# Kernel optimization log

Measured on AMD Instinct MI355X. Metric: run time of the kernel, lower is better.

Reference implementation:

```python
import jax, jax.numpy as jnp
import numpy as np

ALPHA = 1.702
LIMIT = 7.0
TOP_K = 2
B, S, H, E, I = 2, 1024, 768, 8, 768


def setup_inputs() -> dict:
    key = jax.random.key(0)
    ks = jax.random.split(key, 7)
    scale = 0.02
    return {
        "hidden_states": jax.random.normal(ks[0], (B, S, H), dtype=jnp.float32),
        "Wr": jax.random.normal(ks[1], (H, E), dtype=jnp.float32) * scale,
        "br": jax.random.normal(ks[2], (E,), dtype=jnp.float32) * scale,
        "Wgu": jax.random.normal(ks[3], (E, H, 2 * I), dtype=jnp.float32) * scale,
        "bgu": jax.random.normal(ks[4], (E, 2 * I), dtype=jnp.float32) * scale,
        "Wd": jax.random.normal(ks[5], (E, I, H), dtype=jnp.float32) * scale,
        "bd": jax.random.normal(ks[6], (E, H), dtype=jnp.float32) * scale,
    }


def reference(hidden_states, Wr, br, Wgu, bgu, Wd, bd):
    # Router: top-K experts per token, softmax over the K selected logits
    logits = jnp.einsum("bsh,he->bse", hidden_states, Wr) + br
    topk_vals, topk_idx = jax.lax.top_k(logits, TOP_K)        # [B,S,K]
    router_scores = jax.nn.softmax(topk_vals, axis=-1)         # [B,S,K]

    # Dense-over-experts grouped GEMM (sparse_matmul reference: unselected
    # experts are computed but never read by the combine gather below).
    gu = jnp.einsum("bsh,ehf->bsef", hidden_states, Wgu) + bgu  # [B,S,E,2I]
    gu = jnp.minimum(gu, LIMIT)
    gate = gu[..., :I]
    up = jnp.maximum(gu[..., I:], -LIMIT)
    glu = gate * jax.nn.sigmoid(gate * ALPHA)
    activated = (up + 1.0) * glu                                # [B,S,E,I]

    down = jnp.einsum("bsei,eih->bseh", activated, Wd) + bd     # [B,S,E,H]

    # all_to_all_combine (num_devices=1): gather this token's K expert outputs
    sel = jnp.take_along_axis(down, topk_idx[..., None], axis=2)  # [B,S,K,H]
    output = jnp.sum(sel * router_scores[..., None], axis=2)      # [B,S,H]
    return output
```

## Files before the change

kernel.cpp:

```cpp
#include <hip/hip_runtime.h>
#include <hip/hip_bf16.h>
#include <cmath>

#define ALPHA 1.702f
#define LIMIT 7.0f

constexpr int B = 2, S = 1024, H = 768, E = 8, I = 768;
constexpr int T = B * S;
constexpr int TWO_I = 2 * I;
constexpr int CAP = T;
constexpr int NROWS = T * 2;
constexpr int NT1 = I / 64;
constexpr int NT2 = H / 64;
constexpr int MT = CAP / 128;

typedef __attribute__((ext_vector_type(8))) short short8;
typedef __attribute__((ext_vector_type(4))) float floatx4;

__device__ __forceinline__ unsigned short f2bf(float v) {
  __hip_bfloat16 h = __float2bfloat16(v);
  return *reinterpret_cast<unsigned short*>(&h);
}

__device__ __forceinline__ void g2l16(const void* g, void* l) {
  __builtin_amdgcn_global_load_lds(
      (const __attribute__((address_space(1))) void*)g,
      (__attribute__((address_space(3))) void*)l, 16, 0, 0);
}

__global__ __launch_bounds__(64) void router_kernel(
    const float* __restrict__ x, const float* __restrict__ Wr,
    const float* __restrict__ br, int* __restrict__ topk_idx,
    float* __restrict__ topk_w, unsigned short* __restrict__ xb,
    float* __restrict__ out) {
  int t = blockIdx.x;
  int lane = threadIdx.x;
  const float* xr = x + (size_t)t * H;

  float4 z4 = {0.f, 0.f, 0.f, 0.f};
#pragma unroll
  for (int j = 0; j < 3; j++)
    *(float4*)(out + (size_t)t * H + (size_t)(j * 64 + lane) * 4) = z4;

  float acc[E];
#pragma unroll
  for (int e = 0; e < E; e++) acc[e] = 0.0f;

#pragma unroll
  for (int it = 0; it < 3; it++) {
    int h4 = it * 64 + lane;
    float4 xv = *(const float4*)(xr + (size_t)h4 * 4);
    ushort4 xo;
    xo.x = f2bf(xv.x);
    xo.y = f2bf(xv.y);
    xo.z = f2bf(xv.z);
    xo.w = f2bf(xv.w);
    *(ushort4*)(xb + (size_t)t * H + (size_t)h4 * 4) = xo;
    const float* wrow = Wr + (size_t)h4 * 4 * E;
    float xs[4] = {xv.x, xv.y, xv.z, xv.w};
#pragma unroll
    for (int j = 0; j < 4; j++)
#pragma unroll
      for (int e = 0; e < E; e++) acc[e] += xs[j] * wrow[j * E + e];
  }
#pragma unroll
  for (int e = 0; e < E; e++) {
    float v = acc[e];
    for (int off = 32; off > 0; off >>= 1) v += __shfl_down(v, off, 64);
    acc[e] = v;
  }
  if (lane == 0) {
    float logits[E];
#pragma unroll
    for (int e = 0; e < E; e++) logits[e] = acc[e] + br[e];
    int i0 = 0;
    float v0 = logits[0];
#pragma unroll
    for (int e = 1; e < E; e++)
      if (logits[e] > v0) { v0 = logits[e]; i0 = e; }
    int i1 = -1;
    float v1 = -INFINITY;
#pragma unroll
    for (int e = 0; e < E; e++) {
      if (e == i0) continue;
      if (logits[e] > v1) { v1 = logits[e]; i1 = e; }
    }
    float s1 = __expf(v1 - v0);
    float denom = 1.0f + s1;
    topk_idx[t * 2 + 0] = i0;
    topk_idx[t * 2 + 1] = i1;
    topk_w[t * 2 + 0] = 1.0f / denom;
    topk_w[t * 2 + 1] = s1 / denom;
  }
}

__global__ __launch_bounds__(256) void transpose_all(
    const float* __restrict__ Wgu, const float* __restrict__ Wd,
    unsigned short* __restrict__ Wgt, unsigned short* __restrict__ Wdt,
    const int* __restrict__ topk_idx, const float* __restrict__ topk_w,
    int* __restrict__ e_cnt, int* __restrict__ row_token,
    float* __restrict__ row_w) {
  int z = blockIdx.z;
  int tid = threadIdx.x;

  if (z == 16) {
    if (blockIdx.x != 0 || blockIdx.y != 0) return;
    __shared__ int cur[E];
    if (tid < E) cur[tid] = 0;
    __syncthreads();
    for (int i = tid; i < NROWS; i += 256) {
      int e = topk_idx[i];
      int pos = atomicAdd(&cur[e], 1);
      row_token[e * CAP + pos] = i >> 1;
      row_w[e * CAP + pos] = topk_w[i];
    }
    __syncthreads();
    if (tid < E) e_cnt[tid] = cur[tid];
    return;
  }

  int which = z >> 3, e = z & 7;
  int N = which ? H : TWO_I;
  if (which && blockIdx.x >= (H / 64)) return;
  const float* in = which ? (Wd + (size_t)e * H * I)
                          : (Wgu + (size_t)e * H * TWO_I);
  unsigned short* out = which ? (Wdt + (size_t)e * H * I)
                              : (Wgt + (size_t)e * H * TWO_I);
  constexpr int K = 768;
  int n0 = blockIdx.x * 64, k0 = blockIdx.y * 64;

  __shared__ float tile[64][65];
  int jr = tid & 15, r0 = tid >> 4;
#pragma unroll
  for (int p = 0; p < 4; p++) {
    int k = r0 + p * 16;
    float4 v = *(const float4*)(in + (size_t)(k0 + k) * N + n0 + jr * 4);
    tile[k][jr * 4 + 0] = v.x;
    tile[k][jr * 4 + 1] = v.y;
    tile[k][jr * 4 + 2] = v.z;
    tile[k][jr * 4 + 3] = v.w;
  }
  __syncthreads();
#pragma unroll
  for (int p = 0; p < 4; p++) {
    int n = r0 + p * 16;
    ushort4 o;
    o.x = f2bf(tile[jr * 4 + 0][n]);
    o.y = f2bf(tile[jr * 4 + 1][n]);
    o.z = f2bf(tile[jr * 4 + 2][n]);
    o.w = f2bf(tile[jr * 4 + 3][n]);
    *(ushort4*)(out + (size_t)(n0 + n) * K + k0 + jr * 4) = o;
  }
}

__global__ __launch_bounds__(256) void gemm_gu_mfma(
    const unsigned short* __restrict__ xb, const unsigned short* __restrict__ Wgt,
    const float* __restrict__ bgu, const int* __restrict__ e_cnt,
    const int* __restrict__ row_token, unsigned short* __restrict__ act) {
  int bid = blockIdx.x;
  int g = bid % (E * NT1);
  int mt = bid / (E * NT1);
  int e = g / NT1;
  int n0 = (g % NT1) * 64;
  int cnt = e_cnt[e];
  int m0 = mt * 128;
  if (m0 >= cnt) return;
  int start = e * CAP;
  const unsigned short* Wg = Wgt + (size_t)e * TWO_I * H;
  const float* bias = bgu + (size_t)e * TWO_I;

  __shared__ short As[2][128 * 64];
  __shared__ short Bg[2][64 * 64];
  __shared__ short Bu[2][64 * 64];
  __shared__ int tok[128];

  int tid = threadIdx.x;
  if (tid < 128) {
    int m = m0 + tid;
    tok[tid] = row_token[start + ((m < cnt) ? m : (cnt - 1))];
  }
  __syncthreads();

  int lane = tid & 63;
  int wave = tid >> 6;
  int quad = lane >> 4;
  int lrow = lane & 15;
  int wm = (wave >> 1) * 64;
  int wn = (wave & 1) * 32;

  const unsigned short* gA[4];
  int oA[4];
#pragma unroll
  for (int r = 0; r < 4; r++) {
    int s = (wave * 4 + r) * 64 + lane;
    int row = s >> 3;
    int gg = (s & 7) ^ (row & 7);
    gA[r] = xb + (size_t)tok[row] * H + gg * 8;
    oA[r] = (wave * 4 + r) * 64 * 8;
  }
  const unsigned short *gBg[2], *gBu[2];
  int oB[2];
#pragma unroll
  for (int r = 0; r < 2; r++) {
    int s = (wave * 2 + r) * 64 + lane;
    int row = s >> 3;
    int gg = (s & 7) ^ (row & 7);
    gBg[r] = Wg + (size_t)(n0 + row) * H + gg * 8;
    gBu[r] = gBg[r] + (size_t)I * H;
    oB[r] = (wave * 2 + r) * 64 * 8;
  }

  float bgv[2], buv[2];
#pragma unroll
  for (int tj = 0; tj < 2; tj++) {
    int ncol = n0 + wn + tj * 16 + lrow;
    bgv[tj] = bias[ncol];
    buv[tj] = bias[I + ncol];
  }

  floatx4 accg[4][2], accu[4][2];
#pragma unroll
  for (int i = 0; i < 4; i++)
#pragma unroll
    for (int j = 0; j < 2; j++) {
      accg[i][j] = floatx4{0.f, 0.f, 0.f, 0.f};
      accu[i][j] = floatx4{0.f, 0.f, 0.f, 0.f};
    }

  __syncthreads();

#pragma unroll
  for (int r = 0; r < 4; r++) g2l16(gA[r], &As[0][oA[r]]);
#pragma unroll
  for (int r = 0; r < 2; r++) {
    g2l16(gBg[r], &Bg[0][oB[r]]);
    g2l16(gBu[r], &Bu[0][oB[r]]);
  }

  constexpr int NK = H / 64;
  for (int i = 0; i < NK; i++) {
    int cb = i & 1;
    if (i + 1 < NK) {
      int nb = cb ^ 1;
      int k1 = (i + 1) * 64;
#pragma unroll
      for (int r = 0; r < 4; r++) g2l16(gA[r] + k1, &As[nb][oA[r]]);
#pragma unroll
      for (int r = 0; r < 2; r++) {
        g2l16(gBg[r] + k1, &Bg[nb][oB[r]]);
        g2l16(gBu[r] + k1, &Bu[nb][oB[r]]);
      }
      asm volatile("s_waitcnt vmcnt(8)" ::: "memory");
    } else {
      asm volatile("s_waitcnt vmcnt(0)" ::: "memory");
    }
    __builtin_amdgcn_s_barrier();

#pragma unroll
    for (int ks = 0; ks < 2; ks++) {
      int c = ks * 4 + quad;
      short8 a[4], bg[2], bu[2];
#pragma unroll
      for (int ti = 0; ti < 4; ti++) {
        int r = wm + ti * 16 + lrow;
        a[ti] = *(const short8*)(&As[cb][(r * 8 + (c ^ (r & 7))) * 8]);
      }
#pragma unroll
      for (int tj = 0; tj < 2; tj++) {
        int r = wn + tj * 16 + lrow;
        bg[tj] = *(const short8*)(&Bg[cb][(r * 8 + (c ^ (r & 7))) * 8]);
        bu[tj] = *(const short8*)(&Bu[cb][(r * 8 + (c ^ (r & 7))) * 8]);
      }
#pragma unroll
      for (int ti = 0; ti < 4; ti++)
#pragma unroll
        for (int tj = 0; tj < 2; tj++) {
          accg[ti][tj] = __builtin_amdgcn_mfma_f32_16x16x32_bf16(
              a[ti], bg[tj], accg[ti][tj], 0, 0, 0);
          accu[ti][tj] = __builtin_amdgcn_mfma_f32_16x16x32_bf16(
              a[ti], bu[tj], accu[ti][tj], 0, 0, 0);
        }
    }
    __builtin_amdgcn_s_barrier();
  }

#pragma unroll
  for (int ti = 0; ti < 4; ti++) {
#pragma unroll
    for (int tj = 0; tj < 2; tj++) {
      int ncol = n0 + wn + tj * 16 + lrow;
#pragma unroll
      for (int r = 0; r < 4; r++) {
        int m = m0 + wm + ti * 16 + quad * 4 + r;
        if (m < cnt) {
          float gg = accg[ti][tj][r] + bgv[tj];
          float u = accu[ti][tj][r] + buv[tj];
          gg = fminf(gg, LIMIT);
          u = fmaxf(fminf(u, LIMIT), -LIMIT);
          float glu = gg / (1.0f + __expf(-ALPHA * gg));
          act[(size_t)(start + m) * I + ncol] = f2bf((u + 1.0f) * glu);
        }
      }
    }
  }
}

__global__ __launch_bounds__(256) void gemm_down_mfma(
    const unsigned short* __restrict__ act, const unsigned short* __restrict__ Wdt,
    const float* __restrict__ bd, const int* __restrict__ e_cnt,
    const int* __restrict__ row_token, const float* __restrict__ row_w,
    float* __restrict__ out) {
  int bid = blockIdx.x;
  int g = bid % (E * NT2);
  int mt = bid / (E * NT2);
  int e = g / NT2;
  int n0 = (g % NT2) * 64;
  int cnt = e_cnt[e];
  int m0 = mt * 128;
  if (m0 >= cnt) return;
  int start = e * CAP;
  const unsigned short* Wd = Wdt + (size_t)e * H * I;
  const float* bias = bd + (size_t)e * H;

  __shared__ short As[2][128 * 64];
  __shared__ short Bs[2][64 * 64];
  __shared__ int tok[128];
  __shared__ float wts[128];

  int tid = threadIdx.x;
  if (tid < 128) {
    int m = m0 + tid;
    int mm = (m < cnt) ? m : (cnt - 1);
    tok[tid] = row_token[start + mm];
    wts[tid] = row_w[start + mm];
  }
  __syncthreads();

  int lane = tid & 63;
  int wave = tid >> 6;
  int quad = lane >> 4;
  int lrow = lane & 15;
  int wm = (wave >> 1) * 64;
  int wn = (wave & 1) * 32;

  const unsigned short* gA[4];
  int oA[4];
#pragma unroll
  for (int r = 0; r < 4; r++) {
    int s = (wave * 4 + r) * 64 + lane;
    int row = s >> 3;
    int gg = (s & 7) ^ (row & 7);
    int gm = m0 + row;
    int mm = (gm < cnt) ? gm : (cnt - 1);
    gA[r] = act + (size_t)(start + mm) * I + gg * 8;
    oA[r] = (wave * 4 + r) * 64 * 8;
  }
  const unsigned short* gB[2];
  int oB[2];
#pragma unroll
  for (int r = 0; r < 2; r++) {
    int s = (wave * 2 + r) * 64 + lane;
    int row = s >> 3;
    int gg = (s & 7) ^ (row & 7);
    gB[r] = Wd + (size_t)(n0 + row) * I + gg * 8;
    oB[r] = (wave * 2 + r) * 64 * 8;
  }

  float bdv[2];
#pragma unroll
  for (int tj = 0; tj < 2; tj++) bdv[tj] = bias[n0 + wn + tj * 16 + lrow];

  floatx4 acc[4][2];
#pragma unroll
  for (int i = 0; i < 4; i++)
#pragma unroll
    for (int j = 0; j < 2; j++) acc[i][j] = floatx4{0.f, 0.f, 0.f, 0.f};

  __syncthreads();

#pragma unroll
  for (int r = 0; r < 4; r++) g2l16(gA[r], &As[0][oA[r]]);
#pragma unroll
  for (int r = 0; r < 2; r++) g2l16(gB[r], &Bs[0][oB[r]]);

  constexpr int NK = I / 64;
  for (int i = 0; i < NK; i++) {
    int cb = i & 1;
    if (i + 1 < NK) {
      int nb = cb ^ 1;
      int k1 = (i + 1) * 64;
#pragma unroll
      for (int r = 0; r < 4; r++) g2l16(gA[r] + k1, &As[nb][oA[r]]);
#pragma unroll
      for (int r = 0; r < 2; r++) g2l16(gB[r] + k1, &Bs[nb][oB[r]]);
      asm volatile("s_waitcnt vmcnt(6)" ::: "memory");
    } else {
      asm volatile("s_waitcnt vmcnt(0)" ::: "memory");
    }
    __builtin_amdgcn_s_barrier();

#pragma unroll
    for (int ks = 0; ks < 2; ks++) {
      int c = ks * 4 + quad;
      short8 a[4], b[2];
#pragma unroll
      for (int ti = 0; ti < 4; ti++) {
        int r = wm + ti * 16 + lrow;
        a[ti] = *(const short8*)(&As[cb][(r * 8 + (c ^ (r & 7))) * 8]);
      }
#pragma unroll
      for (int tj = 0; tj < 2; tj++) {
        int r = wn + tj * 16 + lrow;
        b[tj] = *(const short8*)(&Bs[cb][(r * 8 + (c ^ (r & 7))) * 8]);
      }
#pragma unroll
      for (int ti = 0; ti < 4; ti++)
#pragma unroll
        for (int tj = 0; tj < 2; tj++)
          acc[ti][tj] = __builtin_amdgcn_mfma_f32_16x16x32_bf16(
              a[ti], b[tj], acc[ti][tj], 0, 0, 0);
    }
    __builtin_amdgcn_s_barrier();
  }

#pragma unroll
  for (int ti = 0; ti < 4; ti++) {
#pragma unroll
    for (int tj = 0; tj < 2; tj++) {
      int ncol = n0 + wn + tj * 16 + lrow;
#pragma unroll
      for (int r = 0; r < 4; r++) {
        int ml = wm + ti * 16 + quad * 4 + r;
        int m = m0 + ml;
        if (m < cnt) {
          atomicAdd(&out[(size_t)tok[ml] * H + ncol],
                    wts[ml] * (acc[ti][tj][r] + bdv[tj]));
        }
      }
    }
  }
}

extern "C" void kernel_launch(void* const* d_in, const int* in_sizes, int n_in,
                              void* d_out, int out_size, void* d_ws,
                              size_t ws_size, hipStream_t stream) {
  const float* x   = (const float*)d_in[0];
  const float* Wr  = (const float*)d_in[1];
  const float* br  = (const float*)d_in[2];
  const float* Wgu = (const float*)d_in[3];
  const float* bgu = (const float*)d_in[4];
  const float* Wd  = (const float*)d_in[5];
  const float* bd  = (const float*)d_in[6];
  float* out = (float*)d_out;

  char* w = (char*)d_ws;
  int* e_cnt = (int*)w;       w += 16 * sizeof(int);
  int* topk_idx = (int*)w;    w += (size_t)T * 2 * sizeof(int);
  float* topk_w = (float*)w;  w += (size_t)T * 2 * sizeof(float);
  int* row_token = (int*)w;   w += (size_t)E * CAP * sizeof(int);
  float* row_w = (float*)w;   w += (size_t)E * CAP * sizeof(float);
  unsigned short* xb  = (unsigned short*)w; w += (size_t)T * H * 2;
  unsigned short* Wgt = (unsigned short*)w; w += (size_t)E * TWO_I * H * 2;
  unsigned short* Wdt = (unsigned short*)w; w += (size_t)E * H * I * 2;
  unsigned short* act = (unsigned short*)w; w += (size_t)E * CAP * I * 2;

  router_kernel<<<T, 64, 0, stream>>>(x, Wr, br, topk_idx, topk_w, xb, out);
  transpose_all<<<dim3(TWO_I / 64, H / 64, 17), 256, 0, stream>>>(
      Wgu, Wd, Wgt, Wdt, topk_idx, topk_w, e_cnt, row_token, row_w);
  gemm_gu_mfma<<<dim3(MT * E * NT1), 256, 0, stream>>>(
      xb, Wgt, bgu, e_cnt, row_token, act);
  gemm_down_mfma<<<dim3(MT * E * NT2), 256, 0, stream>>>(
      act, Wdt, bd, e_cnt, row_token, row_w, out);
}
```

Baseline: 167.0 us.

## Load A operand directly from global into registers, bypassing LDS

In both expert GEMM kernels the activation (A) tile is no longer staged through shared memory. Each wave now loads its MFMA A fragments straight from global memory into a double-buffered register array one K-step ahead. The K loop is fully unrolled and the vmcnt waits are adjusted to the larger number of loads in flight. This removes LDS writes and reads for A and frees shared memory. In exchange it costs more VGPRs, loads A rows twice (once per wave pair sharing rows), and uses less coalesced 64-byte-per-row global accesses.

```diff
diff --git a/kernel.cpp b/kernel.cpp
--- a/kernel.cpp
+++ b/kernel.cpp
@@ -169,7 +169,6 @@
   const unsigned short* Wg = Wgt + (size_t)e * TWO_I * H;
   const float* bias = bgu + (size_t)e * TWO_I;
 
-  __shared__ short As[2][128 * 64];
   __shared__ short Bg[2][64 * 64];
   __shared__ short Bu[2][64 * 64];
   __shared__ int tok[128];
@@ -189,15 +188,12 @@
   int wn = (wave & 1) * 32;
 
   const unsigned short* gA[4];
-  int oA[4];
-#pragma unroll
-  for (int r = 0; r < 4; r++) {
-    int s = (wave * 4 + r) * 64 + lane;
-    int row = s >> 3;
-    int gg = (s & 7) ^ (row & 7);
-    gA[r] = xb + (size_t)tok[row] * H + gg * 8;
-    oA[r] = (wave * 4 + r) * 64 * 8;
-  }
+#pragma unroll
+  for (int ti = 0; ti < 4; ti++) {
+    int row = wm + ti * 16 + lrow;
+    gA[ti] = xb + (size_t)tok[row] * H + quad * 8;
+  }
+
   const unsigned short *gBg[2], *gBu[2];
   int oB[2];
 #pragma unroll
@@ -229,8 +225,12 @@
 
   __syncthreads();
 
-#pragma unroll
-  for (int r = 0; r < 4; r++) g2l16(gA[r], &As[0][oA[r]]);
+  short8 aq[2][2][4];
+#pragma unroll
+  for (int ks = 0; ks < 2; ks++)
+#pragma unroll
+    for (int ti = 0; ti < 4; ti++)
+      aq[0][ks][ti] = *(const short8*)(gA[ti] + ks * 32);
 #pragma unroll
   for (int r = 0; r < 2; r++) {
     g2l16(gBg[r], &Bg[0][oB[r]]);
@@ -238,19 +238,23 @@
   }
 
   constexpr int NK = H / 64;
+#pragma unroll
   for (int i = 0; i < NK; i++) {
     int cb = i & 1;
+    int pc = i & 1, pn = pc ^ 1;
     if (i + 1 < NK) {
-      int nb = cb ^ 1;
       int k1 = (i + 1) * 64;
 #pragma unroll
-      for (int r = 0; r < 4; r++) g2l16(gA[r] + k1, &As[nb][oA[r]]);
+      for (int ks = 0; ks < 2; ks++)
+#pragma unroll
+        for (int ti = 0; ti < 4; ti++)
+          aq[pn][ks][ti] = *(const short8*)(gA[ti] + k1 + ks * 32);
 #pragma unroll
       for (int r = 0; r < 2; r++) {
-        g2l16(gBg[r] + k1, &Bg[nb][oB[r]]);
-        g2l16(gBu[r] + k1, &Bu[nb][oB[r]]);
+        g2l16(gBg[r] + k1, &Bg[cb ^ 1][oB[r]]);
+        g2l16(gBu[r] + k1, &Bu[cb ^ 1][oB[r]]);
       }
-      asm volatile("s_waitcnt vmcnt(8)" ::: "memory");
+      asm volatile("s_waitcnt vmcnt(12)" ::: "memory");
     } else {
       asm volatile("s_waitcnt vmcnt(0)" ::: "memory");
     }
@@ -259,12 +263,7 @@
 #pragma unroll
     for (int ks = 0; ks < 2; ks++) {
       int c = ks * 4 + quad;
-      short8 a[4], bg[2], bu[2];
-#pragma unroll
-      for (int ti = 0; ti < 4; ti++) {
-        int r = wm + ti * 16 + lrow;
-        a[ti] = *(const short8*)(&As[cb][(r * 8 + (c ^ (r & 7))) * 8]);
-      }
+      short8 bg[2], bu[2];
 #pragma unroll
       for (int tj = 0; tj < 2; tj++) {
         int r = wn + tj * 16 + lrow;
@@ -276,9 +275,9 @@
 #pragma unroll
         for (int tj = 0; tj < 2; tj++) {
           accg[ti][tj] = __builtin_amdgcn_mfma_f32_16x16x32_bf16(
-              a[ti], bg[tj], accg[ti][tj], 0, 0, 0);
+              aq[pc][ks][ti], bg[tj], accg[ti][tj], 0, 0, 0);
           accu[ti][tj] = __builtin_amdgcn_mfma_f32_16x16x32_bf16(
-              a[ti], bu[tj], accu[ti][tj], 0, 0, 0);
+              aq[pc][ks][ti], bu[tj], accu[ti][tj], 0, 0, 0);
         }
     }
     __builtin_amdgcn_s_barrier();
@@ -322,7 +321,6 @@
   const unsigned short* Wd = Wdt + (size_t)e * H * I;
   const float* bias = bd + (size_t)e * H;
 
-  __shared__ short As[2][128 * 64];
   __shared__ short Bs[2][64 * 64];
   __shared__ int tok[128];
   __shared__ float wts[128];
@@ -344,17 +342,14 @@
   int wn = (wave & 1) * 32;
 
   const unsigned short* gA[4];
-  int oA[4];
-#pragma unroll
-  for (int r = 0; r < 4; r++) {
-    int s = (wave * 4 + r) * 64 + lane;
-    int row = s >> 3;
-    int gg = (s & 7) ^ (row & 7);
+#pragma unroll
+  for (int ti = 0; ti < 4; ti++) {
+    int row = wm + ti * 16 + lrow;
     int gm = m0 + row;
     int mm = (gm < cnt) ? gm : (cnt - 1);
-    gA[r] = act + (size_t)(start + mm) * I + gg * 8;
-    oA[r] = (wave * 4 + r) * 64 * 8;
-  }
+    gA[ti] = act + (size_t)(start + mm) * I + quad * 8;
+  }
+
   const unsigned short* gB[2];
   int oB[2];
 #pragma unroll
@@ -378,22 +373,30 @@
 
   __syncthreads();
 
-#pragma unroll
-  for (int r = 0; r < 4; r++) g2l16(gA[r], &As[0][oA[r]]);
+  short8 aq[2][2][4];
+#pragma unroll
+  for (int ks = 0; ks < 2; ks++)
+#pragma unroll
+    for (int ti = 0; ti < 4; ti++)
+      aq[0][ks][ti] = *(const short8*)(gA[ti] + ks * 32);
 #pragma unroll
   for (int r = 0; r < 2; r++) g2l16(gB[r], &Bs[0][oB[r]]);
 
   constexpr int NK = I / 64;
+#pragma unroll
   for (int i = 0; i < NK; i++) {
     int cb = i & 1;
+    int pc = i & 1, pn = pc ^ 1;
     if (i + 1 < NK) {
-      int nb = cb ^ 1;
       int k1 = (i + 1) * 64;
 #pragma unroll
-      for (int r = 0; r < 4; r++) g2l16(gA[r] + k1, &As[nb][oA[r]]);
-#pragma unroll
-      for (int r = 0; r < 2; r++) g2l16(gB[r] + k1, &Bs[nb][oB[r]]);
-      asm volatile("s_waitcnt vmcnt(6)" ::: "memory");
+      for (int ks = 0; ks < 2; ks++)
+#pragma unroll
+        for (int ti = 0; ti < 4; ti++)
+          aq[pn][ks][ti] = *(const short8*)(gA[ti] + k1 + ks * 32);
+#pragma unroll
+      for (int r = 0; r < 2; r++) g2l16(gB[r] + k1, &Bs[cb ^ 1][oB[r]]);
+      asm volatile("s_waitcnt vmcnt(10)" ::: "memory");
     } else {
       asm volatile("s_waitcnt vmcnt(0)" ::: "memory");
     }
@@ -402,12 +405,7 @@
 #pragma unroll
     for (int ks = 0; ks < 2; ks++) {
       int c = ks * 4 + quad;
-      short8 a[4], b[2];
-#pragma unroll
-      for (int ti = 0; ti < 4; ti++) {
-        int r = wm + ti * 16 + lrow;
-        a[ti] = *(const short8*)(&As[cb][(r * 8 + (c ^ (r & 7))) * 8]);
-      }
+      short8 b[2];
 #pragma unroll
       for (int tj = 0; tj < 2; tj++) {
         int r = wn + tj * 16 + lrow;
@@ -418,7 +416,7 @@
 #pragma unroll
         for (int tj = 0; tj < 2; tj++)
           acc[ti][tj] = __builtin_amdgcn_mfma_f32_16x16x32_bf16(
-              a[ti], b[tj], acc[ti][tj], 0, 0, 0);
+              aq[pc][ks][ti], b[tj], acc[ti][tj], 0, 0, 0);
     }
     __builtin_amdgcn_s_barrier();
   }
```

New measurement: 190.3 us. 14.0% more time.
